# Kernel optimization log

Hardware: AMD Instinct MI355X
Metric: run time of the kernel (lower is better)

Reference implementation:

```python
import jax, jax.numpy as jnp
import numpy as np

N_HEAD, N_KV_HEAD, N_EMBD, SEQ_LEN = 16, 4, 1024, 2048
HEAD_DIM = N_EMBD // N_HEAD  # 64
B = 2


def _rope(x, cos, sin):
    # x: [B, T, H, D]; cos/sin: [1, T, 1, D//2]
    d = x.shape[-1] // 2
    x1, x2 = x[..., :d], x[..., d:]
    return jnp.concatenate([x1 * cos + x2 * sin, -x1 * sin + x2 * cos], axis=-1)


def setup_inputs() -> dict:
    key = jax.random.key(0)
    ks = jax.random.split(key, 5)
    x = jax.random.normal(ks[0], (B, SEQ_LEN, N_EMBD), dtype=jnp.float32)
    # real RoPE tables (base 10000)
    half = HEAD_DIM // 2
    inv_freq = 1.0 / (10000.0 ** (jnp.arange(half, dtype=jnp.float32) / half))
    ang = jnp.arange(SEQ_LEN, dtype=jnp.float32)[:, None] * inv_freq[None, :]  # [T, half]
    cos = jnp.cos(ang)[None, :, None, :]  # [1, T, 1, half]
    sin = jnp.sin(ang)[None, :, None, :]
    s = 0.02
    Wq = s * jax.random.normal(ks[1], (N_EMBD, N_HEAD * HEAD_DIM), dtype=jnp.float32)
    Wk = s * jax.random.normal(ks[2], (N_EMBD, N_KV_HEAD * HEAD_DIM), dtype=jnp.float32)
    Wv = s * jax.random.normal(ks[3], (N_EMBD, N_KV_HEAD * HEAD_DIM), dtype=jnp.float32)
    Wo = s * jax.random.normal(ks[4], (N_EMBD, N_EMBD), dtype=jnp.float32)
    return {"x": x, "cos": cos, "sin": sin, "Wq": Wq, "Wk": Wk, "Wv": Wv, "Wo": Wo}


def reference(x, cos, sin, Wq, Wk, Wv, Wo):
    Bsz, T, C = x.shape
    H, Hkv, D = N_HEAD, N_KV_HEAD, HEAD_DIM
    q = (x @ Wq).reshape(Bsz, T, H, D)
    k = (x @ Wk).reshape(Bsz, T, Hkv, D)
    v = (x @ Wv).reshape(Bsz, T, Hkv, D)
    q = _rope(q, cos, sin)
    k = _rope(k, cos, sin)
    # GQA: repeat kv heads to match query heads
    rep = H // Hkv
    k = jnp.repeat(k, rep, axis=2)  # [B, T, H, D]
    v = jnp.repeat(v, rep, axis=2)
    scale = 1.0 / np.sqrt(D).astype(np.float32)
    att = jnp.einsum('bqhd,bkhd->bhqk', q, k) * scale  # [B, H, T, T]
    causal = jnp.tril(jnp.ones((T, T), dtype=bool))
    att = jnp.where(causal[None, None, :, :], att, -jnp.inf)
    att = jax.nn.softmax(att, axis=-1)
    y = jnp.einsum('bhqk,bkhd->bqhd', att, v).reshape(Bsz, T, C)
    return y @ Wo
```

## Files before the change

### kernel.cpp

```cpp
#include <hip/hip_runtime.h>
#include <hip/hip_bf16.h>


typedef __attribute__((ext_vector_type(8))) short s16x8;
typedef __attribute__((ext_vector_type(4))) float f32x4;
typedef __attribute__((ext_vector_type(4))) unsigned short u16x4;

#define LOG2E 1.44269504088896340736f

__device__ __forceinline__ float bf2f(unsigned short u) {
  unsigned int i = ((unsigned int)u) << 16;
  return __builtin_bit_cast(float, i);
}
__device__ __forceinline__ unsigned short f2bf(float f) {
  unsigned int i = __builtin_bit_cast(unsigned int, f);
  i += 0x7fffu + ((i >> 16) & 1u);
  return (unsigned short)(i >> 16);
}

__device__ __forceinline__ void async16(const void* g, void* l) {
  __builtin_amdgcn_global_load_lds(
      (const __attribute__((address_space(1))) void*)g,
      (__attribute__((address_space(3))) void*)l, 16, 0, 0);
}


__global__ void conv_f32_to_bf16(const float* __restrict__ in,
                                 unsigned short* __restrict__ out, int n) {
  int i = (blockIdx.x * blockDim.x + threadIdx.x) * 4;
  if (i + 3 < n) {
    float4 v = *(const float4*)(in + i);
    u16x4 o = { f2bf(v.x), f2bf(v.y), f2bf(v.z), f2bf(v.w) };
    *(u16x4*)(out + i) = o;
  }
}

__global__ void transpose_conv(const float* __restrict__ W,
                               unsigned short* __restrict__ Wt, int K, int N) {
  __shared__ float tile[32][33];
  int n0 = blockIdx.x * 32, k0 = blockIdx.y * 32;
  int tx = threadIdx.x, ty = threadIdx.y;
  for (int i = ty; i < 32; i += 8)
    tile[i][tx] = W[(size_t)(k0 + i) * N + n0 + tx];
  __syncthreads();
  for (int i = ty; i < 32; i += 8)
    Wt[(size_t)(n0 + i) * K + k0 + tx] = f2bf(tile[tx][i]);
}

__global__ void rope_qk(unsigned short* __restrict__ QKV,
                        const float* __restrict__ cosb,
                        const float* __restrict__ sinb) {
  int idx = blockIdx.x * blockDim.x + threadIdx.x;
  int d = idx & 31;
  int hh = (idx >> 5) % 20;
  int row = idx / (32 * 20);
  int t = row & 2047;
  size_t base;
  float mul;
  if (hh < 16) { base = (size_t)row * 1536 + hh * 64 + d;               mul = 0.125f; }
  else         { base = (size_t)row * 1536 + 1024 + (hh - 16) * 64 + d; mul = 1.0f;   }
  float x1 = bf2f(QKV[base]), x2 = bf2f(QKV[base + 32]);
  float c = cosb[t * 32 + d], s = sinb[t * 32 + d];
  QKV[base]      = f2bf((x1 * c + x2 * s) * mul);
  QKV[base + 32] = f2bf((-x1 * s + x2 * c) * mul);
}

__global__ __launch_bounds__(256) void gemm_bt(
    const unsigned short* __restrict__ A, const unsigned short* __restrict__ Bt,
    void* __restrict__ Cp, int M, int N, int K, int c_f32) {
  __shared__ unsigned short As[128 * 32];
  __shared__ unsigned short Bs[64 * 32];
  int tid = threadIdx.x;
  int w = tid >> 6, l = tid & 63, g = l >> 4, lr = l & 15;
  int wr = w >> 1, wc = w & 1;
  int m0 = blockIdx.y * 128, n0 = blockIdx.x * 64;
  int sk = lr & 3;

  f32x4 acc[4][2] = {};

  for (int k0 = 0; k0 < K; k0 += 32) {
#pragma unroll
    for (int i = 0; i < 2; ++i) {
      int c = i * 256 + tid;
      int row = c >> 2, srcc = ((c & 3) ^ (row & 3)) * 8;
      async16(A + (size_t)(m0 + row) * K + k0 + srcc, (char*)As + c * 16);
    }
    {
      int c = tid;
      int row = c >> 2, srcc = ((c & 3) ^ (row & 3)) * 8;
      async16(Bt + (size_t)(n0 + row) * K + k0 + srcc, (char*)Bs + c * 16);
    }
    __syncthreads();

    s16x8 af[4], bfr[2];
#pragma unroll
    for (int m = 0; m < 4; ++m)
      af[m] = *(const s16x8*)(As + (wr * 64 + m * 16 + lr) * 32 + (g ^ sk) * 8);
#pragma unroll
    for (int n = 0; n < 2; ++n)
      bfr[n] = *(const s16x8*)(Bs + (wc * 32 + n * 16 + lr) * 32 + (g ^ sk) * 8);
#pragma unroll
    for (int m = 0; m < 4; ++m)
#pragma unroll
      for (int n = 0; n < 2; ++n)
        acc[m][n] = __builtin_amdgcn_mfma_f32_16x16x32_bf16(af[m], bfr[n],
                                                            acc[m][n], 0, 0, 0);
    __syncthreads();
  }

  if (c_f32) {
    float* C = (float*)Cp;
#pragma unroll
    for (int m = 0; m < 4; ++m)
#pragma unroll
      for (int n = 0; n < 2; ++n)
#pragma unroll
        for (int r = 0; r < 4; ++r)
          C[(size_t)(m0 + wr * 64 + m * 16 + g * 4 + r) * N +
            n0 + wc * 32 + n * 16 + lr] = acc[m][n][r];
  } else {
    unsigned short* C = (unsigned short*)Cp;
#pragma unroll
    for (int m = 0; m < 4; ++m)
#pragma unroll
      for (int n = 0; n < 2; ++n)
#pragma unroll
        for (int r = 0; r < 4; ++r)
          C[(size_t)(m0 + wr * 64 + m * 16 + g * 4 + r) * N +
            n0 + wc * 32 + n * 16 + lr] = f2bf(acc[m][n][r]);
  }
}

__global__ __launch_bounds__(256) void attn_fused(
    const unsigned short* __restrict__ QKV, unsigned short* __restrict__ Y) {
  __shared__ unsigned short Kt[2][64 * 64];
  __shared__ unsigned short Vt[2][64 * 64];
  __shared__ unsigned short Pb[4][16 * 64];

  const int T = 2048, CS = 1536;
  int tid = threadIdx.x;
  int w = tid >> 6, l = tid & 63, g = l >> 4, lr = l & 15;
  int n = blockIdx.x;
  int qt = 31 - (n >> 5);
  int bh = n & 31, b = bh >> 4, h = bh & 15, kvh = h >> 2;
  int q0 = qt * 64, qw = q0 + w * 16;
  int sx = lr & 7;
  int q_mine = qw + lr;

  const unsigned short* Qp = QKV + (size_t)b * T * CS + h * 64;
  const unsigned short* Kp = QKV + (size_t)b * T * CS + 1024 + kvh * 64;
  const unsigned short* Vp = QKV + (size_t)b * T * CS + 1280 + kvh * 64;

  s16x8 qf[2];
#pragma unroll
  for (int ks = 0; ks < 2; ++ks)
    qf[ks] = *(const s16x8*)(Qp + (size_t)q_mine * CS + ks * 32 + g * 8);

  f32x4 o[4] = {};
  float mrun = -1e30f, lrun = 0.f;

  unsigned short* Pw = Pb[w];
  int ntiles = qt + 1;

#pragma unroll
  for (int i = 0; i < 2; ++i) {
    int c = i * 256 + tid;
    int row = c >> 3, srcc = ((c & 7) ^ (row & 7)) * 8;
    async16(Kp + (size_t)row * CS + srcc, (char*)(&Kt[0][0]) + c * 16);
  }
#pragma unroll
  for (int i = 0; i < 2; ++i) {
    int c = i * 256 + tid;
    int kv = c & 63, d0v = (c >> 6) * 8;
    s16x8 vv = *(const s16x8*)(Vp + (size_t)kv * CS + d0v);
#pragma unroll
    for (int j = 0; j < 8; ++j)
      Vt[0][(d0v + j) * 64 + (kv ^ (j * 8))] = (unsigned short)vv[j];
  }
  __syncthreads();

  int cur = 0;
  for (int it = 0; it < ntiles; ++it) {
    int kv0 = it * 64;
    bool hasnext = (it + 1 < ntiles);

    s16x8 vvA, vvB;
    int kvA = tid & 63, dA = (tid >> 6) * 8;
    int dB = dA + 32;
    if (hasnext) {
      int kvn = kv0 + 64;
#pragma unroll
      for (int i = 0; i < 2; ++i) {
        int c = i * 256 + tid;
        int row = c >> 3, srcc = ((c & 7) ^ (row & 7)) * 8;
        async16(Kp + (size_t)(kvn + row) * CS + srcc,
                (char*)(&Kt[cur ^ 1][0]) + c * 16);
      }
      vvA = *(const s16x8*)(Vp + (size_t)(kvn + kvA) * CS + dA);
      vvB = *(const s16x8*)(Vp + (size_t)(kvn + kvA) * CS + dB);
    }

    const unsigned short* Kc = &Kt[cur][0];
    const unsigned short* Vc = &Vt[cur][0];
    f32x4 s[4];
    __builtin_amdgcn_s_setprio(1);
#pragma unroll
    for (int nf = 0; nf < 4; ++nf) {
      f32x4 z = {};
#pragma unroll
      for (int ks = 0; ks < 2; ++ks) {
        s16x8 kf = *(const s16x8*)(Kc + (nf * 16 + lr) * 64 +
                                   ((ks * 4 + g) ^ sx) * 8);
        z = __builtin_amdgcn_mfma_f32_16x16x32_bf16(kf, qf[ks], z, 0, 0, 0);
      }
      s[nf] = z;
    }
    __builtin_amdgcn_s_setprio(0);

    if (it == ntiles - 1) {
#pragma unroll
      for (int nf = 0; nf < 4; ++nf)
#pragma unroll
        for (int r = 0; r < 4; ++r)
          if (kv0 + nf * 16 + g * 4 + r > q_mine) s[nf][r] = -1e30f;
    }

    float mt = s[0][0];
#pragma unroll
    for (int nf = 0; nf < 4; ++nf)
#pragma unroll
      for (int r = 0; r < 4; ++r) mt = fmaxf(mt, s[nf][r]);
    mt = fmaxf(mt, __shfl_xor(mt, 16, 64));
    mt = fmaxf(mt, __shfl_xor(mt, 32, 64));

    if (__any(mt > mrun + 8.f)) {
      float mnew = fmaxf(mrun, mt);
      float corr = exp2f((mrun - mnew) * LOG2E);
      float psum = 0.f;
#pragma unroll
      for (int nf = 0; nf < 4; ++nf)
#pragma unroll
        for (int r = 0; r < 4; ++r) {
          float p = exp2f((s[nf][r] - mnew) * LOG2E);
          s[nf][r] = p;
          psum += p;
        }
      psum += __shfl_xor(psum, 16, 64);
      psum += __shfl_xor(psum, 32, 64);
      lrun = lrun * corr + psum;
      mrun = mnew;
#pragma unroll
      for (int r = 0; r < 4; ++r) {
        float cr = __shfl(corr, g * 4 + r, 64);
#pragma unroll
        for (int d0 = 0; d0 < 4; ++d0) o[d0][r] *= cr;
      }
    } else {
      float psum = 0.f;
#pragma unroll
      for (int nf = 0; nf < 4; ++nf)
#pragma unroll
        for (int r = 0; r < 4; ++r) {
          float p = exp2f((s[nf][r] - mrun) * LOG2E);
          s[nf][r] = p;
          psum += p;
        }
      psum += __shfl_xor(psum, 16, 64);
      psum += __shfl_xor(psum, 32, 64);
      lrun += psum;
    }

#pragma unroll
    for (int nf = 0; nf < 4; ++nf)
#pragma unroll
      for (int r = 0; r < 4; ++r) {
        int col = nf * 16 + g * 4 + r;
        Pw[lr * 64 + (col ^ (sx * 8))] = f2bf(s[nf][r]);
      }
    asm volatile("s_waitcnt lgkmcnt(0)" ::: "memory");
    __builtin_amdgcn_sched_barrier(0);

    s16x8 pf[2];
#pragma unroll
    for (int ks = 0; ks < 2; ++ks)
      pf[ks] = *(const s16x8*)(Pw + lr * 64 + ((ks * 4 + g) ^ sx) * 8);
    __builtin_amdgcn_s_setprio(1);
#pragma unroll
    for (int d0 = 0; d0 < 4; ++d0)
#pragma unroll
      for (int ks = 0; ks < 2; ++ks) {
        s16x8 vf = *(const s16x8*)(Vc + (d0 * 16 + lr) * 64 +
                                   ((ks * 4 + g) ^ sx) * 8);
        o[d0] = __builtin_amdgcn_mfma_f32_16x16x32_bf16(pf[ks], vf, o[d0], 0, 0, 0);
      }
    __builtin_amdgcn_s_setprio(0);

    if (hasnext) {
#pragma unroll
      for (int j = 0; j < 8; ++j)
        Vt[cur ^ 1][(dA + j) * 64 + (kvA ^ (j * 8))] = (unsigned short)vvA[j];
#pragma unroll
      for (int j = 0; j < 8; ++j)
        Vt[cur ^ 1][(dB + j) * 64 + (kvA ^ (j * 8))] = (unsigned short)vvB[j];
    }
    __syncthreads();
    cur ^= 1;
  }

#pragma unroll
  for (int r = 0; r < 4; ++r) {
    float lv = __shfl(lrun, g * 4 + r, 64);
    float inv = 1.f / lv;
    size_t rowoff = (size_t)(b * T + qw + g * 4 + r) * 1024 + h * 64;
#pragma unroll
    for (int d0 = 0; d0 < 4; ++d0)
      Y[rowoff + d0 * 16 + lr] = f2bf(o[d0][r] * inv);
  }
}


extern "C" void kernel_launch(void* const* d_in, const int* in_sizes, int n_in,
                              void* d_out, int out_size, void* d_ws, size_t ws_size,
                              hipStream_t stream) {
  const float* x    = (const float*)d_in[0];
  const float* cosb = (const float*)d_in[1];
  const float* sinb = (const float*)d_in[2];
  const float* Wq   = (const float*)d_in[3];
  const float* Wk   = (const float*)d_in[4];
  const float* Wv   = (const float*)d_in[5];
  const float* Wo   = (const float*)d_in[6];
  float* out = (float*)d_out;

  char* ob = (char*)d_out;
  char* ws = (char*)d_ws;
  const size_t MB = 1024 * 1024;
  unsigned short* QKVb  = (unsigned short*)(ob);
  unsigned short* xb    = (unsigned short*)(ws);
  unsigned short* Wqkvt = (unsigned short*)(ws + 8 * MB);
  unsigned short* Wot   = (unsigned short*)(ws + 11 * MB);
  unsigned short* Yb    = xb;

  conv_f32_to_bf16<<<4096, 256, 0, stream>>>(x, xb, 4096 * 1024);
  transpose_conv<<<dim3(32, 32), dim3(32, 8), 0, stream>>>(Wq, Wqkvt, 1024, 1024);
  transpose_conv<<<dim3(8, 32), dim3(32, 8), 0, stream>>>(Wk, Wqkvt + (size_t)1024 * 1024, 1024, 256);
  transpose_conv<<<dim3(8, 32), dim3(32, 8), 0, stream>>>(Wv, Wqkvt + (size_t)1280 * 1024, 1024, 256);
  transpose_conv<<<dim3(32, 32), dim3(32, 8), 0, stream>>>(Wo, Wot, 1024, 1024);

  gemm_bt<<<dim3(24, 32), 256, 0, stream>>>(xb, Wqkvt, QKVb, 4096, 1536, 1024, 0);

  rope_qk<<<10240, 256, 0, stream>>>(QKVb, cosb, sinb);

  attn_fused<<<dim3(1024), 256, 0, stream>>>(QKVb, Yb);

  gemm_bt<<<dim3(16, 32), 256, 0, stream>>>(Yb, Wot, out, 4096, 1024, 1024, 1);
}
```

Baseline: 142.1 us.

## Pair causal query tiles per attention block and widen GEMM K-tile

Each attention block now handles two query tiles, a long one (31-ip) and a short one (ip), so every block does the same number of KV iterations and causal load imbalance disappears. The grid is halved to 512 blocks to match. The GEMM K-step grows from 32 to 64 with a matching 8-way swizzle, which halves the number of barriers per block but doubles LDS use. P stores to LDS are vectorised as 4-wide writes. With 512 blocks of 4 waves, fewer waves may be resident per CU to hide latency.

```diff
diff --git a/kernel.cpp b/kernel.cpp
--- a/kernel.cpp
+++ b/kernel.cpp
@@ -68,43 +68,51 @@
 __global__ __launch_bounds__(256) void gemm_bt(
     const unsigned short* __restrict__ A, const unsigned short* __restrict__ Bt,
     void* __restrict__ Cp, int M, int N, int K, int c_f32) {
-  __shared__ unsigned short As[128 * 32];
-  __shared__ unsigned short Bs[64 * 32];
+  __shared__ unsigned short As[128 * 64];
+  __shared__ unsigned short Bs[64 * 64];
   int tid = threadIdx.x;
   int w = tid >> 6, l = tid & 63, g = l >> 4, lr = l & 15;
   int wr = w >> 1, wc = w & 1;
   int m0 = blockIdx.y * 128, n0 = blockIdx.x * 64;
-  int sk = lr & 3;
+  int sk = lr & 7;
 
   f32x4 acc[4][2] = {};
 
-  for (int k0 = 0; k0 < K; k0 += 32) {
+  for (int k0 = 0; k0 < K; k0 += 64) {
+#pragma unroll
+    for (int i = 0; i < 4; ++i) {
+      int c = i * 256 + tid;
+      int row = c >> 3, srcu = ((c & 7) ^ (row & 7)) * 8;
+      async16(A + (size_t)(m0 + row) * K + k0 + srcu, (char*)As + c * 16);
+    }
 #pragma unroll
     for (int i = 0; i < 2; ++i) {
       int c = i * 256 + tid;
-      int row = c >> 2, srcc = ((c & 3) ^ (row & 3)) * 8;
-      async16(A + (size_t)(m0 + row) * K + k0 + srcc, (char*)As + c * 16);
-    }
-    {
-      int c = tid;
-      int row = c >> 2, srcc = ((c & 3) ^ (row & 3)) * 8;
-      async16(Bt + (size_t)(n0 + row) * K + k0 + srcc, (char*)Bs + c * 16);
+      int row = c >> 3, srcu = ((c & 7) ^ (row & 7)) * 8;
+      async16(Bt + (size_t)(n0 + row) * K + k0 + srcu, (char*)Bs + c * 16);
     }
     __syncthreads();
 
-    s16x8 af[4], bfr[2];
-#pragma unroll
-    for (int m = 0; m < 4; ++m)
-      af[m] = *(const s16x8*)(As + (wr * 64 + m * 16 + lr) * 32 + (g ^ sk) * 8);
-#pragma unroll
-    for (int n = 0; n < 2; ++n)
-      bfr[n] = *(const s16x8*)(Bs + (wc * 32 + n * 16 + lr) * 32 + (g ^ sk) * 8);
-#pragma unroll
-    for (int m = 0; m < 4; ++m)
+    s16x8 af[2][4], bfr[2][2];
+#pragma unroll
+    for (int ks = 0; ks < 2; ++ks) {
+#pragma unroll
+      for (int m = 0; m < 4; ++m)
+        af[ks][m] = *(const s16x8*)(As + (wr * 64 + m * 16 + lr) * 64 +
+                                    ((ks * 4 + g) ^ sk) * 8);
 #pragma unroll
       for (int n = 0; n < 2; ++n)
-        acc[m][n] = __builtin_amdgcn_mfma_f32_16x16x32_bf16(af[m], bfr[n],
-                                                            acc[m][n], 0, 0, 0);
+        bfr[ks][n] = *(const s16x8*)(Bs + (wc * 32 + n * 16 + lr) * 64 +
+                                     ((ks * 4 + g) ^ sk) * 8);
+    }
+#pragma unroll
+    for (int ks = 0; ks < 2; ++ks)
+#pragma unroll
+      for (int m = 0; m < 4; ++m)
+#pragma unroll
+        for (int n = 0; n < 2; ++n)
+          acc[m][n] = __builtin_amdgcn_mfma_f32_16x16x32_bf16(
+              af[ks][m], bfr[ks][n], acc[m][n], 0, 0, 0);
     __syncthreads();
   }
 
@@ -141,180 +149,182 @@
   int tid = threadIdx.x;
   int w = tid >> 6, l = tid & 63, g = l >> 4, lr = l & 15;
   int n = blockIdx.x;
-  int qt = 31 - (n >> 5);
+  int ip = n >> 5;
   int bh = n & 31, b = bh >> 4, h = bh & 15, kvh = h >> 2;
-  int q0 = qt * 64, qw = q0 + w * 16;
   int sx = lr & 7;
-  int q_mine = qw + lr;
 
   const unsigned short* Qp = QKV + (size_t)b * T * CS + h * 64;
   const unsigned short* Kp = QKV + (size_t)b * T * CS + 1024 + kvh * 64;
   const unsigned short* Vp = QKV + (size_t)b * T * CS + 1280 + kvh * 64;
-
-  s16x8 qf[2];
-#pragma unroll
-  for (int ks = 0; ks < 2; ++ks)
-    qf[ks] = *(const s16x8*)(Qp + (size_t)q_mine * CS + ks * 32 + g * 8);
-
-  f32x4 o[4] = {};
-  float mrun = -1e30f, lrun = 0.f;
-
   unsigned short* Pw = Pb[w];
-  int ntiles = qt + 1;
-
-#pragma unroll
-  for (int i = 0; i < 2; ++i) {
-    int c = i * 256 + tid;
-    int row = c >> 3, srcc = ((c & 7) ^ (row & 7)) * 8;
-    async16(Kp + (size_t)row * CS + srcc, (char*)(&Kt[0][0]) + c * 16);
-  }
-#pragma unroll
-  for (int i = 0; i < 2; ++i) {
-    int c = i * 256 + tid;
-    int kv = c & 63, d0v = (c >> 6) * 8;
-    s16x8 vv = *(const s16x8*)(Vp + (size_t)kv * CS + d0v);
-#pragma unroll
-    for (int j = 0; j < 8; ++j)
-      Vt[0][(d0v + j) * 64 + (kv ^ (j * 8))] = (unsigned short)vv[j];
-  }
-  __syncthreads();
-
-  int cur = 0;
-  for (int it = 0; it < ntiles; ++it) {
-    int kv0 = it * 64;
-    bool hasnext = (it + 1 < ntiles);
-
-    s16x8 vvA, vvB;
-    int kvA = tid & 63, dA = (tid >> 6) * 8;
-    int dB = dA + 32;
-    if (hasnext) {
-      int kvn = kv0 + 64;
-#pragma unroll
-      for (int i = 0; i < 2; ++i) {
-        int c = i * 256 + tid;
-        int row = c >> 3, srcc = ((c & 7) ^ (row & 7)) * 8;
-        async16(Kp + (size_t)(kvn + row) * CS + srcc,
-                (char*)(&Kt[cur ^ 1][0]) + c * 16);
-      }
-      vvA = *(const s16x8*)(Vp + (size_t)(kvn + kvA) * CS + dA);
-      vvB = *(const s16x8*)(Vp + (size_t)(kvn + kvA) * CS + dB);
-    }
-
-    const unsigned short* Kc = &Kt[cur][0];
-    const unsigned short* Vc = &Vt[cur][0];
-    f32x4 s[4];
-    __builtin_amdgcn_s_setprio(1);
-#pragma unroll
-    for (int nf = 0; nf < 4; ++nf) {
-      f32x4 z = {};
-#pragma unroll
-      for (int ks = 0; ks < 2; ++ks) {
-        s16x8 kf = *(const s16x8*)(Kc + (nf * 16 + lr) * 64 +
-                                   ((ks * 4 + g) ^ sx) * 8);
-        z = __builtin_amdgcn_mfma_f32_16x16x32_bf16(kf, qf[ks], z, 0, 0, 0);
-      }
-      s[nf] = z;
-    }
-    __builtin_amdgcn_s_setprio(0);
-
-    if (it == ntiles - 1) {
+
+  int kvA = tid & 63, dA = (tid >> 6) * 8, dB = dA + 32;
+
+  for (int pass = 0; pass < 2; ++pass) {
+    int qt = pass == 0 ? (31 - ip) : ip;
+    int qw = qt * 64 + w * 16;
+    int q_mine = qw + lr;
+
+    s16x8 qf[2];
+#pragma unroll
+    for (int ks = 0; ks < 2; ++ks)
+      qf[ks] = *(const s16x8*)(Qp + (size_t)q_mine * CS + ks * 32 + g * 8);
+
+    f32x4 o[4] = {};
+    float mrun = -1e30f, lrun = 0.f;
+    int ntiles = qt + 1;
+
+#pragma unroll
+    for (int i = 0; i < 2; ++i) {
+      int c = i * 256 + tid;
+      int row = c >> 3, srcc = ((c & 7) ^ (row & 7)) * 8;
+      async16(Kp + (size_t)row * CS + srcc, (char*)(&Kt[0][0]) + c * 16);
+    }
+#pragma unroll
+    for (int i = 0; i < 2; ++i) {
+      int c = i * 256 + tid;
+      int kv = c & 63, d0v = (c >> 6) * 8;
+      s16x8 vv = *(const s16x8*)(Vp + (size_t)kv * CS + d0v);
+#pragma unroll
+      for (int j = 0; j < 8; ++j)
+        Vt[0][(d0v + j) * 64 + (kv ^ (j * 8))] = (unsigned short)vv[j];
+    }
+    __syncthreads();
+
+    int cur = 0;
+    for (int it = 0; it < ntiles; ++it) {
+      int kv0 = it * 64;
+      bool hasnext = (it + 1 < ntiles);
+
+      s16x8 vvA, vvB;
+      if (hasnext) {
+        int kvn = kv0 + 64;
+#pragma unroll
+        for (int i = 0; i < 2; ++i) {
+          int c = i * 256 + tid;
+          int row = c >> 3, srcc = ((c & 7) ^ (row & 7)) * 8;
+          async16(Kp + (size_t)(kvn + row) * CS + srcc,
+                  (char*)(&Kt[cur ^ 1][0]) + c * 16);
+        }
+        vvA = *(const s16x8*)(Vp + (size_t)(kvn + kvA) * CS + dA);
+        vvB = *(const s16x8*)(Vp + (size_t)(kvn + kvA) * CS + dB);
+      }
+
+      const unsigned short* Kc = &Kt[cur][0];
+      const unsigned short* Vc = &Vt[cur][0];
+      f32x4 s[4];
+      __builtin_amdgcn_s_setprio(1);
+#pragma unroll
+      for (int nf = 0; nf < 4; ++nf) {
+        f32x4 z = {};
+#pragma unroll
+        for (int ks = 0; ks < 2; ++ks) {
+          s16x8 kf = *(const s16x8*)(Kc + (nf * 16 + lr) * 64 +
+                                     ((ks * 4 + g) ^ sx) * 8);
+          z = __builtin_amdgcn_mfma_f32_16x16x32_bf16(kf, qf[ks], z, 0, 0, 0);
+        }
+        s[nf] = z;
+      }
+      __builtin_amdgcn_s_setprio(0);
+
+      if (it == ntiles - 1) {
+#pragma unroll
+        for (int nf = 0; nf < 4; ++nf)
+#pragma unroll
+          for (int r = 0; r < 4; ++r)
+            if (kv0 + nf * 16 + g * 4 + r > q_mine) s[nf][r] = -1e30f;
+      }
+
+      float mt = s[0][0];
 #pragma unroll
       for (int nf = 0; nf < 4; ++nf)
 #pragma unroll
-        for (int r = 0; r < 4; ++r)
-          if (kv0 + nf * 16 + g * 4 + r > q_mine) s[nf][r] = -1e30f;
-    }
-
-    float mt = s[0][0];
-#pragma unroll
-    for (int nf = 0; nf < 4; ++nf)
-#pragma unroll
-      for (int r = 0; r < 4; ++r) mt = fmaxf(mt, s[nf][r]);
-    mt = fmaxf(mt, __shfl_xor(mt, 16, 64));
-    mt = fmaxf(mt, __shfl_xor(mt, 32, 64));
-
-    if (__any(mt > mrun + 8.f)) {
-      float mnew = fmaxf(mrun, mt);
-      float corr = exp2f((mrun - mnew) * LOG2E);
-      float psum = 0.f;
-#pragma unroll
-      for (int nf = 0; nf < 4; ++nf)
+        for (int r = 0; r < 4; ++r) mt = fmaxf(mt, s[nf][r]);
+      mt = fmaxf(mt, __shfl_xor(mt, 16, 64));
+      mt = fmaxf(mt, __shfl_xor(mt, 32, 64));
+
+      if (__any(mt > mrun + 8.f)) {
+        float mnew = fmaxf(mrun, mt);
+        float corr = exp2f((mrun - mnew) * LOG2E);
+        float psum = 0.f;
+#pragma unroll
+        for (int nf = 0; nf < 4; ++nf)
+#pragma unroll
+          for (int r = 0; r < 4; ++r) {
+            float p = exp2f((s[nf][r] - mnew) * LOG2E);
+            s[nf][r] = p;
+            psum += p;
+          }
+        psum += __shfl_xor(psum, 16, 64);
+        psum += __shfl_xor(psum, 32, 64);
+        lrun = lrun * corr + psum;
+        mrun = mnew;
 #pragma unroll
         for (int r = 0; r < 4; ++r) {
-          float p = exp2f((s[nf][r] - mnew) * LOG2E);
-          s[nf][r] = p;
-          psum += p;
+          float cr = __shfl(corr, g * 4 + r, 64);
+#pragma unroll
+          for (int d0 = 0; d0 < 4; ++d0) o[d0][r] *= cr;
         }
-      psum += __shfl_xor(psum, 16, 64);
-      psum += __shfl_xor(psum, 32, 64);
-      lrun = lrun * corr + psum;
-      mrun = mnew;
-#pragma unroll
-      for (int r = 0; r < 4; ++r) {
-        float cr = __shfl(corr, g * 4 + r, 64);
-#pragma unroll
-        for (int d0 = 0; d0 < 4; ++d0) o[d0][r] *= cr;
-      }
-    } else {
-      float psum = 0.f;
-#pragma unroll
-      for (int nf = 0; nf < 4; ++nf)
-#pragma unroll
-        for (int r = 0; r < 4; ++r) {
-          float p = exp2f((s[nf][r] - mrun) * LOG2E);
-          s[nf][r] = p;
-          psum += p;
+      } else {
+        float psum = 0.f;
+#pragma unroll
+        for (int nf = 0; nf < 4; ++nf)
+#pragma unroll
+          for (int r = 0; r < 4; ++r) {
+            float p = exp2f((s[nf][r] - mrun) * LOG2E);
+            s[nf][r] = p;
+            psum += p;
+          }
+        psum += __shfl_xor(psum, 16, 64);
+        psum += __shfl_xor(psum, 32, 64);
+        lrun += psum;
+      }
+
+#pragma unroll
+      for (int nf = 0; nf < 4; ++nf) {
+        u16x4 pv = { f2bf(s[nf][0]), f2bf(s[nf][1]),
+                     f2bf(s[nf][2]), f2bf(s[nf][3]) };
+        *(u16x4*)(Pw + lr * 64 + ((nf * 16 + g * 4) ^ (sx * 8))) = pv;
+      }
+      asm volatile("s_waitcnt lgkmcnt(0)" ::: "memory");
+      __builtin_amdgcn_sched_barrier(0);
+
+      s16x8 pf[2];
+#pragma unroll
+      for (int ks = 0; ks < 2; ++ks)
+        pf[ks] = *(const s16x8*)(Pw + lr * 64 + ((ks * 4 + g) ^ sx) * 8);
+      __builtin_amdgcn_s_setprio(1);
+#pragma unroll
+      for (int d0 = 0; d0 < 4; ++d0)
+#pragma unroll
+        for (int ks = 0; ks < 2; ++ks) {
+          s16x8 vf = *(const s16x8*)(Vc + (d0 * 16 + lr) * 64 +
+                                     ((ks * 4 + g) ^ sx) * 8);
+          o[d0] = __builtin_amdgcn_mfma_f32_16x16x32_bf16(pf[ks], vf, o[d0], 0, 0, 0);
         }
-      psum += __shfl_xor(psum, 16, 64);
-      psum += __shfl_xor(psum, 32, 64);
-      lrun += psum;
-    }
-
-#pragma unroll
-    for (int nf = 0; nf < 4; ++nf)
-#pragma unroll
-      for (int r = 0; r < 4; ++r) {
-        int col = nf * 16 + g * 4 + r;
-        Pw[lr * 64 + (col ^ (sx * 8))] = f2bf(s[nf][r]);
-      }
-    asm volatile("s_waitcnt lgkmcnt(0)" ::: "memory");
-    __builtin_amdgcn_sched_barrier(0);
-
-    s16x8 pf[2];
-#pragma unroll
-    for (int ks = 0; ks < 2; ++ks)
-      pf[ks] = *(const s16x8*)(Pw + lr * 64 + ((ks * 4 + g) ^ sx) * 8);
-    __builtin_amdgcn_s_setprio(1);
-#pragma unroll
-    for (int d0 = 0; d0 < 4; ++d0)
-#pragma unroll
-      for (int ks = 0; ks < 2; ++ks) {
-        s16x8 vf = *(const s16x8*)(Vc + (d0 * 16 + lr) * 64 +
-                                   ((ks * 4 + g) ^ sx) * 8);
-        o[d0] = __builtin_amdgcn_mfma_f32_16x16x32_bf16(pf[ks], vf, o[d0], 0, 0, 0);
-      }
-    __builtin_amdgcn_s_setprio(0);
-
-    if (hasnext) {
-#pragma unroll
-      for (int j = 0; j < 8; ++j)
-        Vt[cur ^ 1][(dA + j) * 64 + (kvA ^ (j * 8))] = (unsigned short)vvA[j];
-#pragma unroll
-      for (int j = 0; j < 8; ++j)
-        Vt[cur ^ 1][(dB + j) * 64 + (kvA ^ (j * 8))] = (unsigned short)vvB[j];
-    }
-    __syncthreads();
-    cur ^= 1;
-  }
-
-#pragma unroll
-  for (int r = 0; r < 4; ++r) {
-    float lv = __shfl(lrun, g * 4 + r, 64);
-    float inv = 1.f / lv;
-    size_t rowoff = (size_t)(b * T + qw + g * 4 + r) * 1024 + h * 64;
-#pragma unroll
-    for (int d0 = 0; d0 < 4; ++d0)
-      Y[rowoff + d0 * 16 + lr] = f2bf(o[d0][r] * inv);
+      __builtin_amdgcn_s_setprio(0);
+
+      if (hasnext) {
+#pragma unroll
+        for (int j = 0; j < 8; ++j)
+          Vt[cur ^ 1][(dA + j) * 64 + (kvA ^ (j * 8))] = (unsigned short)vvA[j];
+#pragma unroll
+        for (int j = 0; j < 8; ++j)
+          Vt[cur ^ 1][(dB + j) * 64 + (kvA ^ (j * 8))] = (unsigned short)vvB[j];
+      }
+      __syncthreads();
+      cur ^= 1;
+    }
+
+#pragma unroll
+    for (int r = 0; r < 4; ++r) {
+      float lv = __shfl(lrun, g * 4 + r, 64);
+      float inv = 1.f / lv;
+      size_t rowoff = (size_t)(b * T + qw + g * 4 + r) * 1024 + h * 64;
+#pragma unroll
+      for (int d0 = 0; d0 < 4; ++d0)
+        Y[rowoff + d0 * 16 + lr] = f2bf(o[d0][r] * inv);
+    }
   }
 }
 
@@ -350,7 +360,7 @@
 
   rope_qk<<<10240, 256, 0, stream>>>(QKVb, cosb, sinb);
 
-  attn_fused<<<dim3(1024), 256, 0, stream>>>(QKVb, Yb);
+  attn_fused<<<dim3(512), 256, 0, stream>>>(QKVb, Yb);
 
   gemm_bt<<<dim3(16, 32), 256, 0, stream>>>(Yb, Wot, out, 4096, 1024, 1024, 1);
 }
```

New measurement: 132.7 us. -6.6%, faster.
